# Optimization experiments

Hardware: AMD Instinct MI355X
Metric: run time of the kernel (lower is better)

The kernel has to match this reference:

```python
import jax, jax.numpy as jnp
import numpy as np

HIDDEN = 2048
NUM_Q_HEADS = 32
NUM_KV_HEADS = 8
HEAD_DIM = HIDDEN // NUM_Q_HEADS  # 64
GROUPS = NUM_Q_HEADS // NUM_KV_HEADS  # 4
MAX_WAVELENGTH = 10000.0
B, S = 2, 1024
NEG_INF = -1e9  # keras Softmax masking constant


def apply_rope(x, start_index=0, max_wavelength=MAX_WAVELENGTH):
    # x: [b, s, h, d]; keras_hub RotaryEmbedding (split-half / Llama style)
    d = x.shape[-1]
    s = x.shape[1]
    freq_range = jnp.arange(0, d, 2, dtype=jnp.float32)
    inverse_freq = 1.0 / (max_wavelength ** (freq_range / d))  # [d/2]
    positions = jnp.arange(s, dtype=jnp.float32) + start_index
    freq = positions[:, None] * inverse_freq[None, :]  # [s, d/2]
    emb = jnp.concatenate([freq, freq], axis=-1)[None, :, None, :]  # [1,s,1,d]
    cos = jnp.cos(emb).astype(x.dtype)
    sin = jnp.sin(emb).astype(x.dtype)
    x1, x2 = jnp.split(x, 2, axis=-1)
    half_rot = jnp.concatenate([-x2, x1], axis=-1)
    return x * cos + half_rot * sin


def setup_inputs() -> dict:
    key = jax.random.key(0)
    k1, k2, k3, k4, k5 = jax.random.split(key, 5)
    hidden_states = jax.random.normal(k1, (B, S, HIDDEN), dtype=jnp.float32)
    # causal mask, broadcast over batch
    attention_mask = jnp.broadcast_to(
        jnp.tril(jnp.ones((S, S), dtype=bool))[None], (B, S, S)
    )
    scale = 1.0 / np.sqrt(HIDDEN)
    Wq = jax.random.normal(k2, (HIDDEN, NUM_Q_HEADS * HEAD_DIM), dtype=jnp.float32) * scale
    Wk = jax.random.normal(k3, (HIDDEN, NUM_KV_HEADS * HEAD_DIM), dtype=jnp.float32) * scale
    Wv = jax.random.normal(k4, (HIDDEN, NUM_KV_HEADS * HEAD_DIM), dtype=jnp.float32) * scale
    Wo = jax.random.normal(k5, (NUM_Q_HEADS * HEAD_DIM, HIDDEN), dtype=jnp.float32) * scale
    return {"hidden_states": hidden_states, "attention_mask": attention_mask,
            "Wq": Wq, "Wk": Wk, "Wv": Wv, "Wo": Wo}


def reference(hidden_states, attention_mask, Wq, Wk, Wv, Wo):
    b, s, _ = hidden_states.shape
    q = (hidden_states @ Wq).reshape(b, s, NUM_Q_HEADS, HEAD_DIM)
    k = (hidden_states @ Wk).reshape(b, s, NUM_KV_HEADS, HEAD_DIM)
    v = (hidden_states @ Wv).reshape(b, s, NUM_KV_HEADS, HEAD_DIM)
    q = apply_rope(q)
    k = apply_rope(k)
    # GQA: repeat kv heads to match query heads (ops.repeat on axis 2)
    k = jnp.repeat(k, GROUPS, axis=2)
    v = jnp.repeat(v, GROUPS, axis=2)
    inv_norm = 1.0 / np.sqrt(HEAD_DIM)
    scores = jnp.einsum("bquh,bkuh->buqk", q, k) * inv_norm  # [b, h, q, k]
    scores = scores.astype(jnp.float32)
    scores = jnp.where(attention_mask[:, None, :, :], scores, NEG_INF)
    probs = jax.nn.softmax(scores, axis=-1).astype(hidden_states.dtype)
    attn = jnp.einsum("buqk,bkuh->bquh", probs, v)  # [b, q, h, hd]
    attn = attn.reshape(b, s, HIDDEN)
    return attn @ Wo
```

## Files before the change

kernel.cpp:

```cpp
#include <hip/hip_runtime.h>
#include <hip/hip_bf16.h>
#include <math.h>

#define S_LEN 1024
#define BATCH 2
#define HIDDEN 2048
#define NQH 32
#define NKVH 8
#define HD 64
#define LDQKV 3072
#define M_ROWS (BATCH * S_LEN)

typedef __attribute__((ext_vector_type(8))) short bf16x8;
typedef __attribute__((ext_vector_type(4))) float f32x4;

typedef unsigned int uint32_g __attribute__((address_space(1)));
typedef unsigned int uint32_l __attribute__((address_space(3)));

static __device__ __forceinline__ void load_lds16(const void* g, void* l) {
    __builtin_amdgcn_global_load_lds((const uint32_g*)g, (uint32_l*)l, 16, 0, 0);
}

static __device__ __forceinline__ short f2bf(float f) {
    union { __hip_bfloat16 h; short s; } cv;
    cv.h = __float2bfloat16(f);
    return cv.s;
}

__global__ __launch_bounds__(256) void conv_all_kernel(
    const float* __restrict__ X,
    const float* __restrict__ Wq, const float* __restrict__ Wk,
    const float* __restrict__ Wv, const float* __restrict__ Wo,
    short* __restrict__ Xb, short* __restrict__ Wqkvt, short* __restrict__ Wot,
    float2* __restrict__ cs2)
{
    __shared__ short Ts[64][68];
    const int tid = threadIdx.x;

    if (blockIdx.z == 4) {
        int flat = blockIdx.y * 32 + blockIdx.x;
        size_t base = (size_t)flat * 4096 + (size_t)tid * 16;
        #pragma unroll
        for (int rep = 0; rep < 2; ++rep) {
            size_t i = base + rep * 8;
            float4 a = *reinterpret_cast<const float4*>(X + i);
            float4 b = *reinterpret_cast<const float4*>(X + i + 4);
            union { bf16x8 v; short s[8]; } t;
            t.s[0] = f2bf(a.x); t.s[1] = f2bf(a.y); t.s[2] = f2bf(a.z); t.s[3] = f2bf(a.w);
            t.s[4] = f2bf(b.x); t.s[5] = f2bf(b.y); t.s[6] = f2bf(b.z); t.s[7] = f2bf(b.w);
            *reinterpret_cast<bf16x8*>(Xb + i) = t.v;
        }
        if (flat < 128) {
            int g = flat * 256 + tid;
            int s = g >> 5, i = g & 31;
            float inv_freq = 1.0f / powf(10000.0f, (float)i / 32.0f);
            float freq = (float)s * inv_freq;
            double sn, cs;
            sincos((double)freq, &sn, &cs);
            cs2[g] = make_float2((float)cs, (float)sn);
        }
        return;
    }

    const float* src; short* dst; int N;
    switch (blockIdx.z) {
        case 0: src = Wq; dst = Wqkvt;                         N = 2048; break;
        case 1: src = Wk; dst = Wqkvt + (size_t)2048 * 2048;   N = 512;  break;
        case 2: src = Wv; dst = Wqkvt + (size_t)2560 * 2048;   N = 512;  break;
        default: src = Wo; dst = Wot;                          N = 2048; break;
    }
    const int n0 = blockIdx.x * 64, k0 = blockIdx.y * 64;
    if (n0 >= N) return;

    #pragma unroll
    for (int rep = 0; rep < 4; ++rep) {
        int idx = rep * 256 + tid;
        int row = idx >> 4, c4 = (idx & 15) * 4;
        float4 v = *reinterpret_cast<const float4*>(
            src + (size_t)(k0 + row) * N + n0 + c4);
        ushort4 u;
        u.x = (unsigned short)f2bf(v.x); u.y = (unsigned short)f2bf(v.y);
        u.z = (unsigned short)f2bf(v.z); u.w = (unsigned short)f2bf(v.w);
        *reinterpret_cast<ushort4*>(&Ts[row][c4]) = u;
    }
    __syncthreads();
    #pragma unroll
    for (int rep = 0; rep < 2; ++rep) {
        int idx = rep * 256 + tid;
        int n = idx >> 3, kc = (idx & 7) * 8;
        union { bf16x8 v; short s[8]; } t;
        #pragma unroll
        for (int j = 0; j < 8; ++j) t.s[j] = Ts[kc + j][n];
        *reinterpret_cast<bf16x8*>(dst + (size_t)(n0 + n) * 2048 + k0 + kc) = t.v;
    }
}

template <bool ROPE_BF16>
__global__ __launch_bounds__(256) void gemm_bf16_kernel(
    const short* __restrict__ A, const short* __restrict__ Bt,
    float* __restrict__ C, short* __restrict__ Cb,
    short* __restrict__ vt_g,
    const float2* __restrict__ cs2, int K, int ldc)
{
    const int n0 = blockIdx.x * 64, m0 = blockIdx.y * 128;
    const int tid = threadIdx.x;
    const int w = tid >> 6, lane = tid & 63;
    const int m15 = lane & 15, q4 = lane >> 4;

    __shared__ short SL[128 * 64 + 64 * 64];
    short (*As)[64] = (short(*)[64])SL;
    short (*Bs)[64] = (short(*)[64])(SL + 128 * 64);

    f32x4 acc[2][4];
    #pragma unroll
    for (int i = 0; i < 2; ++i)
        #pragma unroll
        for (int j = 0; j < 4; ++j) acc[i][j] = (f32x4){0.f, 0.f, 0.f, 0.f};

    const int srow = lane >> 3;
    const int pchunk = lane & 7;

    for (int k0 = 0; k0 < K; k0 += 64) {
        __syncthreads();
        #pragma unroll
        for (int r = 0; r < 4; ++r) {
            int row = (w * 4 + r) * 8 + srow;
            int lchunk = pchunk ^ (row & 7);
            load_lds16(A + (size_t)(m0 + row) * K + k0 + lchunk * 8,
                       &As[(w * 4 + r) * 8][0]);
        }
        #pragma unroll
        for (int r = 0; r < 2; ++r) {
            int row = (w * 2 + r) * 8 + srow;
            int lchunk = pchunk ^ (row & 7);
            load_lds16(Bt + (size_t)(n0 + row) * K + k0 + lchunk * 8,
                       &Bs[(w * 2 + r) * 8][0]);
        }
        __syncthreads();

        #pragma unroll
        for (int ch = 0; ch < 2; ++ch) {
            bf16x8 af[2], bf[4];
            #pragma unroll
            for (int mt = 0; mt < 2; ++mt) {
                int row = w * 32 + mt * 16 + m15;
                af[mt] = *reinterpret_cast<const bf16x8*>(
                    &As[row][(((ch * 4 + q4) ^ (row & 7))) * 8]);
            }
            #pragma unroll
            for (int nt = 0; nt < 4; ++nt) {
                int row = nt * 16 + m15;
                bf[nt] = *reinterpret_cast<const bf16x8*>(
                    &Bs[row][(((ch * 4 + q4) ^ (row & 7))) * 8]);
            }
            #pragma unroll
            for (int mt = 0; mt < 2; ++mt)
                #pragma unroll
                for (int nt = 0; nt < 4; ++nt)
                    acc[mt][nt] = __builtin_amdgcn_mfma_f32_16x16x32_bf16(
                        af[mt], bf[nt], acc[mt][nt], 0, 0, 0);
        }
    }

    if (!ROPE_BF16) {
        #pragma unroll
        for (int mt = 0; mt < 2; ++mt)
            #pragma unroll
            for (int nt = 0; nt < 4; ++nt)
                #pragma unroll
                for (int reg = 0; reg < 4; ++reg)
                    C[(size_t)(m0 + w * 32 + mt * 16 + q4 * 4 + reg) * ldc
                      + n0 + nt * 16 + m15] = acc[mt][nt][reg];
    } else if (n0 < 2560) {
        #pragma unroll
        for (int mt = 0; mt < 2; ++mt) {
            #pragma unroll
            for (int reg = 0; reg < 4; ++reg) {
                int row = m0 + w * 32 + mt * 16 + q4 * 4 + reg;
                int s = row & (S_LEN - 1);
                float2 t0 = cs2[s * 32 + m15];
                float2 t1 = cs2[s * 32 + 16 + m15];
                float a0 = acc[mt][0][reg], a1 = acc[mt][1][reg];
                float a2 = acc[mt][2][reg], a3 = acc[mt][3][reg];
                size_t base = (size_t)row * ldc + n0 + m15;
                Cb[base +  0] = f2bf(a0 * t0.x - a2 * t0.y);
                Cb[base + 16] = f2bf(a1 * t1.x - a3 * t1.y);
                Cb[base + 32] = f2bf(a2 * t0.x + a0 * t0.y);
                Cb[base + 48] = f2bf(a3 * t1.x + a1 * t1.y);
            }
        }
    } else {
        __syncthreads();
        short (*VT)[136] = (short(*)[136])SL;
        #pragma unroll
        for (int mt = 0; mt < 2; ++mt) {
            #pragma unroll
            for (int nt = 0; nt < 4; ++nt) {
                ushort4 u;
                u.x = (unsigned short)f2bf(acc[mt][nt][0]);
                u.y = (unsigned short)f2bf(acc[mt][nt][1]);
                u.z = (unsigned short)f2bf(acc[mt][nt][2]);
                u.w = (unsigned short)f2bf(acc[mt][nt][3]);
                *reinterpret_cast<ushort4*>(
                    &VT[nt * 16 + m15][w * 32 + mt * 16 + q4 * 4]) = u;
            }
        }
        __syncthreads();
        const int kvh = (n0 - 2560) >> 6;
        const int b = m0 >> 10, k0loc = m0 & (S_LEN - 1);
        const int dim = tid >> 2, kc = (tid & 3) * 32;
        short* dst = vt_g + (size_t)((b * 8 + kvh) * 64 + dim) * S_LEN + k0loc + kc;
        #pragma unroll
        for (int u = 0; u < 4; ++u)
            *reinterpret_cast<bf16x8*>(dst + u * 8) =
                *reinterpret_cast<const bf16x8*>(&VT[dim][kc + u * 8]);
    }
}

__global__ __launch_bounds__(256) void attn_kernel(
    const short* __restrict__ qkvb, const short* __restrict__ vt_g,
    short* __restrict__ attn_b)
{
    const int i  = blockIdx.x;
    const int h  = blockIdx.y;
    const int b  = blockIdx.z;
    const int qtA = i;
    const int qtB = 15 - i;
    const int tid = threadIdx.x;
    const int w = tid >> 6, lane = tid & 63;
    const int kvh = h >> 2;
    const int m15 = lane & 15, q4 = lane >> 4;

    __shared__ short Ks[2][64][64];
    __shared__ short Vt[2][64][64];
    __shared__ float Ps[4][16][68];

    const int rowbaseA = qtA * 64 + w * 16;
    const int rowbaseB = qtB * 64 + w * 16;

    const bf16x8 qfA0 = *reinterpret_cast<const bf16x8*>(
        qkvb + (size_t)(b * S_LEN + rowbaseA + m15) * LDQKV + h * HD + q4 * 8);
    const bf16x8 qfA1 = *reinterpret_cast<const bf16x8*>(
        qkvb + (size_t)(b * S_LEN + rowbaseA + m15) * LDQKV + h * HD + 32 + q4 * 8);
    const bf16x8 qfB0 = *reinterpret_cast<const bf16x8*>(
        qkvb + (size_t)(b * S_LEN + rowbaseB + m15) * LDQKV + h * HD + q4 * 8);
    const bf16x8 qfB1 = *reinterpret_cast<const bf16x8*>(
        qkvb + (size_t)(b * S_LEN + rowbaseB + m15) * LDQKV + h * HD + 32 + q4 * 8);

    f32x4 o4A[4], o4B[4];
    #pragma unroll
    for (int k = 0; k < 4; ++k) {
        o4A[k] = (f32x4){0.f, 0.f, 0.f, 0.f};
        o4B[k] = (f32x4){0.f, 0.f, 0.f, 0.f};
    }
    float lsumA[4] = {0.f, 0.f, 0.f, 0.f};
    float lsumB[4] = {0.f, 0.f, 0.f, 0.f};

    const int r8 = lane >> 3, p8 = lane & 7;
    const int lch = (p8 ^ r8) * 8;
    const short* kbase = qkvb + (size_t)(b * S_LEN) * LDQKV + 2048 + kvh * HD;
    const short* vbase = vt_g + (size_t)(b * 8 + kvh) * 64 * S_LEN;

#define STAGE(bf, t) do {                                                     \
    int row0_ = w * 16 + r8, row1_ = w * 16 + 8 + r8;                         \
    load_lds16(kbase + (size_t)((t) * 64 + row0_) * LDQKV + lch,              \
               &Ks[bf][w * 16][0]);                                           \
    load_lds16(kbase + (size_t)((t) * 64 + row1_) * LDQKV + lch,              \
               &Ks[bf][w * 16 + 8][0]);                                       \
    load_lds16(vbase + (size_t)row0_ * S_LEN + (t) * 64 + lch,                \
               &Vt[bf][w * 16][0]);                                           \
    load_lds16(vbase + (size_t)row1_ * S_LEN + (t) * 64 + lch,                \
               &Vt[bf][w * 16 + 8][0]);                                       \
} while (0)

#define COMPUTE(qf0, qf1, rowbase, o4, lsum, bf, t) do {                      \
    const int xr_ = m15 & 7;                                                  \
    bf16x8 pf_[2];                                                            \
    _Pragma("unroll")                                                         \
    for (int nt = 0; nt < 4; ++nt) {                                          \
        f32x4 acc = (f32x4){0.f, 0.f, 0.f, 0.f};                              \
        bf16x8 kf0 = *reinterpret_cast<const bf16x8*>(                        \
            &Ks[bf][nt * 16 + m15][(q4 ^ xr_) * 8]);                          \
        bf16x8 kf1 = *reinterpret_cast<const bf16x8*>(                        \
            &Ks[bf][nt * 16 + m15][((4 + q4) ^ xr_) * 8]);                    \
        acc = __builtin_amdgcn_mfma_f32_16x16x32_bf16(qf0, kf0, acc, 0, 0, 0);\
        acc = __builtin_amdgcn_mfma_f32_16x16x32_bf16(qf1, kf1, acc, 0, 0, 0);\
        int colg = (t) * 64 + nt * 16 + m15;                                  \
        _Pragma("unroll")                                                     \
        for (int reg = 0; reg < 4; ++reg) {                                   \
            int rowg = (rowbase) + q4 * 4 + reg;                              \
            float p = (colg <= rowg)                                          \
                ? exp2f(fminf(acc[reg] * 0.180336880f, 80.f)) : 0.f;          \
            (lsum)[reg] += p;                                                 \
            Ps[w][q4 * 4 + reg][nt * 16 + m15] = p;                           \
        }                                                                     \
    }                                                                         \
    _Pragma("unroll")                                                         \
    for (int ch = 0; ch < 2; ++ch) {                                          \
        f32x4 pa = *reinterpret_cast<const f32x4*>(                           \
            &Ps[w][m15][ch * 32 + q4 * 8]);                                   \
        f32x4 pb = *reinterpret_cast<const f32x4*>(                           \
            &Ps[w][m15][ch * 32 + q4 * 8 + 4]);                               \
        union { bf16x8 v; short s[8]; } tb;                                   \
        tb.s[0] = f2bf(pa[0]); tb.s[1] = f2bf(pa[1]);                         \
        tb.s[2] = f2bf(pa[2]); tb.s[3] = f2bf(pa[3]);                         \
        tb.s[4] = f2bf(pb[0]); tb.s[5] = f2bf(pb[1]);                         \
        tb.s[6] = f2bf(pb[2]); tb.s[7] = f2bf(pb[3]);                         \
        pf_[ch] = tb.v;                                                       \
    }                                                                         \
    _Pragma("unroll")                                                         \
    for (int nt2 = 0; nt2 < 4; ++nt2) {                                       \
        bf16x8 vf0 = *reinterpret_cast<const bf16x8*>(                        \
            &Vt[bf][nt2 * 16 + m15][(q4 ^ xr_) * 8]);                         \
        bf16x8 vf1 = *reinterpret_cast<const bf16x8*>(                        \
            &Vt[bf][nt2 * 16 + m15][((4 + q4) ^ xr_) * 8]);                   \
        (o4)[nt2] = __builtin_amdgcn_mfma_f32_16x16x32_bf16(                  \
            pf_[0], vf0, (o4)[nt2], 0, 0, 0);                                 \
        (o4)[nt2] = __builtin_amdgcn_mfma_f32_16x16x32_bf16(                  \
            pf_[1], vf1, (o4)[nt2], 0, 0, 0);                                 \
    }                                                                         \
} while (0)

    STAGE(0, 0);
    __syncthreads();

    for (int t = 0; t <= qtB; ++t) {
        const int bf = t & 1;
        if (t < qtB) STAGE(bf ^ 1, t + 1);
        if (t <= qtA) COMPUTE(qfA0, qfA1, rowbaseA, o4A, lsumA, bf, t);
        COMPUTE(qfB0, qfB1, rowbaseB, o4B, lsumB, bf, t);
        __syncthreads();
    }

#undef STAGE
#undef COMPUTE

    float invlA[4], invlB[4];
    #pragma unroll
    for (int reg = 0; reg < 4; ++reg) {
        float la = lsumA[reg], lb = lsumB[reg];
        la += __shfl_xor(la, 1, 64);
        la += __shfl_xor(la, 2, 64);
        la += __shfl_xor(la, 4, 64);
        la += __shfl_xor(la, 8, 64);
        lb += __shfl_xor(lb, 1, 64);
        lb += __shfl_xor(lb, 2, 64);
        lb += __shfl_xor(lb, 4, 64);
        lb += __shfl_xor(lb, 8, 64);
        invlA[reg] = 1.0f / la;
        invlB[reg] = 1.0f / lb;
    }

    #pragma unroll
    for (int nt2 = 0; nt2 < 4; ++nt2)
        #pragma unroll
        for (int reg = 0; reg < 4; ++reg) {
            attn_b[(size_t)(b * S_LEN + rowbaseA + q4 * 4 + reg) * HIDDEN
                   + h * HD + nt2 * 16 + m15] = f2bf(o4A[nt2][reg] * invlA[reg]);
            attn_b[(size_t)(b * S_LEN + rowbaseB + q4 * 4 + reg) * HIDDEN
                   + h * HD + nt2 * 16 + m15] = f2bf(o4B[nt2][reg] * invlB[reg]);
        }
}

extern "C" void kernel_launch(void* const* d_in, const int* in_sizes, int n_in,
                              void* d_out, int out_size, void* d_ws, size_t ws_size,
                              hipStream_t stream) {
    const float* X  = (const float*)d_in[0];
    const float* Wq = (const float*)d_in[2];
    const float* Wk = (const float*)d_in[3];
    const float* Wv = (const float*)d_in[4];
    const float* Wo = (const float*)d_in[5];
    float* out = (float*)d_out;

    short*  qkvb  = (short*)d_ws;
    short*  Xb    = qkvb + (size_t)M_ROWS * LDQKV;
    short*  Wqkvt = Xb + (size_t)HIDDEN * HIDDEN;
    short*  Wot   = Wqkvt + (size_t)LDQKV * HIDDEN;
    short*  vt_g  = Wot + (size_t)HIDDEN * HIDDEN;
    float2* cs2   = (float2*)(vt_g + (size_t)16 * 64 * S_LEN);
    short*  attn_b = Xb;

    conv_all_kernel<<<dim3(32, 32, 5), dim3(256), 0, stream>>>(
        X, Wq, Wk, Wv, Wo, Xb, Wqkvt, Wot, cs2);

    gemm_bf16_kernel<true><<<dim3(48, 16), dim3(256), 0, stream>>>(
        Xb, Wqkvt, nullptr, qkvb, vt_g, cs2, 2048, LDQKV);
    attn_kernel<<<dim3(8, 32, 2), dim3(256), 0, stream>>>(qkvb, vt_g, attn_b);
    gemm_bf16_kernel<false><<<dim3(32, 16), dim3(256), 0, stream>>>(
        attn_b, Wot, out, nullptr, nullptr, nullptr, 2048, HIDDEN);
}
```

Baseline: 207.5 us.

## Split paired query tiles across separate waves with 512-thread attention blocks

The attention kernel now launches 512 threads per block. Waves 0-3 handle the long causal tile qtB and waves 4-7 handle the short tile qtA, instead of each wave computing both tiles one after the other. K/V staging is spread over all eight waves, one row chunk each, and Ps grows to eight per-wave slices. This roughly halves per-wave register state and serial MFMA work, giving more waves per CU for latency hiding. The cost is that the qtA waves sit idle at barriers once their tile finishes, and the larger block uses more LDS.

Measured after the change: 205.3 us. Within noise of the previous version (-1.0%).

```diff
diff --git a/kernel.cpp b/kernel.cpp
--- a/kernel.cpp
+++ b/kernel.cpp
@@ -217,7 +217,7 @@
     }
 }
 
-__global__ __launch_bounds__(256) void attn_kernel(
+__global__ __launch_bounds__(512) void attn_kernel(
     const short* __restrict__ qkvb, const short* __restrict__ vt_g,
     short* __restrict__ attn_b)
 {
@@ -233,65 +233,53 @@
 
     __shared__ short Ks[2][64][64];
     __shared__ short Vt[2][64][64];
-    __shared__ float Ps[4][16][68];
-
-    const int rowbaseA = qtA * 64 + w * 16;
-    const int rowbaseB = qtB * 64 + w * 16;
-
-    const bf16x8 qfA0 = *reinterpret_cast<const bf16x8*>(
-        qkvb + (size_t)(b * S_LEN + rowbaseA + m15) * LDQKV + h * HD + q4 * 8);
-    const bf16x8 qfA1 = *reinterpret_cast<const bf16x8*>(
-        qkvb + (size_t)(b * S_LEN + rowbaseA + m15) * LDQKV + h * HD + 32 + q4 * 8);
-    const bf16x8 qfB0 = *reinterpret_cast<const bf16x8*>(
-        qkvb + (size_t)(b * S_LEN + rowbaseB + m15) * LDQKV + h * HD + q4 * 8);
-    const bf16x8 qfB1 = *reinterpret_cast<const bf16x8*>(
-        qkvb + (size_t)(b * S_LEN + rowbaseB + m15) * LDQKV + h * HD + 32 + q4 * 8);
-
-    f32x4 o4A[4], o4B[4];
-    #pragma unroll
-    for (int k = 0; k < 4; ++k) {
-        o4A[k] = (f32x4){0.f, 0.f, 0.f, 0.f};
-        o4B[k] = (f32x4){0.f, 0.f, 0.f, 0.f};
-    }
-    float lsumA[4] = {0.f, 0.f, 0.f, 0.f};
-    float lsumB[4] = {0.f, 0.f, 0.f, 0.f};
+    __shared__ float Ps[8][16][68];
+
+    const int qt_w = (w < 4) ? qtB : qtA;
+    const int rowbase = qt_w * 64 + (w & 3) * 16;
+
+    const bf16x8 qf0 = *reinterpret_cast<const bf16x8*>(
+        qkvb + (size_t)(b * S_LEN + rowbase + m15) * LDQKV + h * HD + q4 * 8);
+    const bf16x8 qf1 = *reinterpret_cast<const bf16x8*>(
+        qkvb + (size_t)(b * S_LEN + rowbase + m15) * LDQKV + h * HD + 32 + q4 * 8);
+
+    f32x4 o4[4];
+    #pragma unroll
+    for (int k = 0; k < 4; ++k) o4[k] = (f32x4){0.f, 0.f, 0.f, 0.f};
+    float lsum[4] = {0.f, 0.f, 0.f, 0.f};
 
     const int r8 = lane >> 3, p8 = lane & 7;
     const int lch = (p8 ^ r8) * 8;
     const short* kbase = qkvb + (size_t)(b * S_LEN) * LDQKV + 2048 + kvh * HD;
     const short* vbase = vt_g + (size_t)(b * 8 + kvh) * 64 * S_LEN;
 
-#define STAGE(bf, t) do {                                                     \
-    int row0_ = w * 16 + r8, row1_ = w * 16 + 8 + r8;                         \
-    load_lds16(kbase + (size_t)((t) * 64 + row0_) * LDQKV + lch,              \
-               &Ks[bf][w * 16][0]);                                           \
-    load_lds16(kbase + (size_t)((t) * 64 + row1_) * LDQKV + lch,              \
-               &Ks[bf][w * 16 + 8][0]);                                       \
-    load_lds16(vbase + (size_t)row0_ * S_LEN + (t) * 64 + lch,                \
-               &Vt[bf][w * 16][0]);                                           \
-    load_lds16(vbase + (size_t)row1_ * S_LEN + (t) * 64 + lch,                \
-               &Vt[bf][w * 16 + 8][0]);                                       \
+#define STAGE(bf_, t) do {                                                    \
+    int row_ = w * 8 + r8;                                                    \
+    load_lds16(kbase + (size_t)((t) * 64 + row_) * LDQKV + lch,               \
+               &Ks[bf_][w * 8][0]);                                           \
+    load_lds16(vbase + (size_t)row_ * S_LEN + (t) * 64 + lch,                 \
+               &Vt[bf_][w * 8][0]);                                           \
 } while (0)
 
-#define COMPUTE(qf0, qf1, rowbase, o4, lsum, bf, t) do {                      \
+#define COMPUTE(bf_, t) do {                                                  \
     const int xr_ = m15 & 7;                                                  \
     bf16x8 pf_[2];                                                            \
     _Pragma("unroll")                                                         \
     for (int nt = 0; nt < 4; ++nt) {                                          \
         f32x4 acc = (f32x4){0.f, 0.f, 0.f, 0.f};                              \
         bf16x8 kf0 = *reinterpret_cast<const bf16x8*>(                        \
-            &Ks[bf][nt * 16 + m15][(q4 ^ xr_) * 8]);                          \
+            &Ks[bf_][nt * 16 + m15][(q4 ^ xr_) * 8]);                         \
         bf16x8 kf1 = *reinterpret_cast<const bf16x8*>(                        \
-            &Ks[bf][nt * 16 + m15][((4 + q4) ^ xr_) * 8]);                    \
+            &Ks[bf_][nt * 16 + m15][((4 + q4) ^ xr_) * 8]);                   \
         acc = __builtin_amdgcn_mfma_f32_16x16x32_bf16(qf0, kf0, acc, 0, 0, 0);\
         acc = __builtin_amdgcn_mfma_f32_16x16x32_bf16(qf1, kf1, acc, 0, 0, 0);\
         int colg = (t) * 64 + nt * 16 + m15;                                  \
         _Pragma("unroll")                                                     \
         for (int reg = 0; reg < 4; ++reg) {                                   \
-            int rowg = (rowbase) + q4 * 4 + reg;                              \
+            int rowg = rowbase + q4 * 4 + reg;                                \
             float p = (colg <= rowg)                                          \
                 ? exp2f(fminf(acc[reg] * 0.180336880f, 80.f)) : 0.f;          \
-            (lsum)[reg] += p;                                                 \
+            lsum[reg] += p;                                                   \
             Ps[w][q4 * 4 + reg][nt * 16 + m15] = p;                           \
         }                                                                     \
     }                                                                         \
@@ -311,13 +299,13 @@
     _Pragma("unroll")                                                         \
     for (int nt2 = 0; nt2 < 4; ++nt2) {                                       \
         bf16x8 vf0 = *reinterpret_cast<const bf16x8*>(                        \
-            &Vt[bf][nt2 * 16 + m15][(q4 ^ xr_) * 8]);                         \
+            &Vt[bf_][nt2 * 16 + m15][(q4 ^ xr_) * 8]);                        \
         bf16x8 vf1 = *reinterpret_cast<const bf16x8*>(                        \
-            &Vt[bf][nt2 * 16 + m15][((4 + q4) ^ xr_) * 8]);                   \
-        (o4)[nt2] = __builtin_amdgcn_mfma_f32_16x16x32_bf16(                  \
-            pf_[0], vf0, (o4)[nt2], 0, 0, 0);                                 \
-        (o4)[nt2] = __builtin_amdgcn_mfma_f32_16x16x32_bf16(                  \
-            pf_[1], vf1, (o4)[nt2], 0, 0, 0);                                 \
+            &Vt[bf_][nt2 * 16 + m15][((4 + q4) ^ xr_) * 8]);                  \
+        o4[nt2] = __builtin_amdgcn_mfma_f32_16x16x32_bf16(                    \
+            pf_[0], vf0, o4[nt2], 0, 0, 0);                                   \
+        o4[nt2] = __builtin_amdgcn_mfma_f32_16x16x32_bf16(                    \
+            pf_[1], vf1, o4[nt2], 0, 0, 0);                                   \
     }                                                                         \
 } while (0)
 
@@ -327,39 +315,30 @@
     for (int t = 0; t <= qtB; ++t) {
         const int bf = t & 1;
         if (t < qtB) STAGE(bf ^ 1, t + 1);
-        if (t <= qtA) COMPUTE(qfA0, qfA1, rowbaseA, o4A, lsumA, bf, t);
-        COMPUTE(qfB0, qfB1, rowbaseB, o4B, lsumB, bf, t);
+        if (t <= qt_w) COMPUTE(bf, t);
         __syncthreads();
     }
 
 #undef STAGE
 #undef COMPUTE
 
-    float invlA[4], invlB[4];
+    float invl[4];
     #pragma unroll
     for (int reg = 0; reg < 4; ++reg) {
-        float la = lsumA[reg], lb = lsumB[reg];
-        la += __shfl_xor(la, 1, 64);
-        la += __shfl_xor(la, 2, 64);
-        la += __shfl_xor(la, 4, 64);
-        la += __shfl_xor(la, 8, 64);
-        lb += __shfl_xor(lb, 1, 64);
-        lb += __shfl_xor(lb, 2, 64);
-        lb += __shfl_xor(lb, 4, 64);
-        lb += __shfl_xor(lb, 8, 64);
-        invlA[reg] = 1.0f / la;
-        invlB[reg] = 1.0f / lb;
+        float l = lsum[reg];
+        l += __shfl_xor(l, 1, 64);
+        l += __shfl_xor(l, 2, 64);
+        l += __shfl_xor(l, 4, 64);
+        l += __shfl_xor(l, 8, 64);
+        invl[reg] = 1.0f / l;
     }
 
     #pragma unroll
     for (int nt2 = 0; nt2 < 4; ++nt2)
         #pragma unroll
-        for (int reg = 0; reg < 4; ++reg) {
-            attn_b[(size_t)(b * S_LEN + rowbaseA + q4 * 4 + reg) * HIDDEN
-                   + h * HD + nt2 * 16 + m15] = f2bf(o4A[nt2][reg] * invlA[reg]);
-            attn_b[(size_t)(b * S_LEN + rowbaseB + q4 * 4 + reg) * HIDDEN
-                   + h * HD + nt2 * 16 + m15] = f2bf(o4B[nt2][reg] * invlB[reg]);
-        }
+        for (int reg = 0; reg < 4; ++reg)
+            attn_b[(size_t)(b * S_LEN + rowbase + q4 * 4 + reg) * HIDDEN
+                   + h * HD + nt2 * 16 + m15] = f2bf(o4[nt2][reg] * invl[reg]);
 }
 
 extern "C" void kernel_launch(void* const* d_in, const int* in_sizes, int n_in,
@@ -385,7 +364,7 @@
 
     gemm_bf16_kernel<true><<<dim3(48, 16), dim3(256), 0, stream>>>(
         Xb, Wqkvt, nullptr, qkvb, vt_g, cs2, 2048, LDQKV);
-    attn_kernel<<<dim3(8, 32, 2), dim3(256), 0, stream>>>(qkvb, vt_g, attn_b);
+    attn_kernel<<<dim3(8, 32, 2), dim3(512), 0, stream>>>(qkvb, vt_g, attn_b);
     gemm_bf16_kernel<false><<<dim3(32, 16), dim3(256), 0, stream>>>(
         attn_b, Wot, out, nullptr, nullptr, nullptr, 2048, HIDDEN);
 }
```
